# Optimization experiments

Hardware: AMD Instinct MI355X
Metric: run time of the kernel (lower is better)

The kernel has to match this reference:

```python
import jax, jax.numpy as jnp
import numpy as np

CAPACITY = 0.125


def setup_inputs() -> dict:
    key = jax.random.key(0)
    ks = jax.random.split(key, 6)
    b, s, d, dff = 4, 8192, 512, 2048
    x = jax.random.normal(ks[0], (b, s, d), dtype=jnp.float32)
    position_ids = jnp.tile(jnp.arange(s, dtype=jnp.int64)[None, :], (b, 1))
    Wr = jax.random.normal(ks[1], (d,), dtype=jnp.float32) * 0.02
    br = jnp.zeros((1,), dtype=jnp.float32)
    W1 = jax.random.normal(ks[2], (d, dff), dtype=jnp.float32) * 0.02
    b1 = jnp.zeros((dff,), dtype=jnp.float32)
    W2 = jax.random.normal(ks[3], (dff, d), dtype=jnp.float32) * 0.02
    b2 = jnp.zeros((d,), dtype=jnp.float32)
    return {"x": x, "position_ids": position_ids, "Wr": Wr, "br": br,
            "W1": W1, "b1": b1, "W2": W2, "b2": b2}


def reference(x, position_ids, Wr, br, W1, b1, W2, b2):
    b, s, d = x.shape
    # Router: Linear(d, 1) -> squeeze(-1)
    weights = jnp.einsum('bsd,d->bs', x, Wr) + br  # [b, s]
    k = int(CAPACITY * s)
    # Per-batch top-k threshold (k-th largest value)
    top_k_values = jax.lax.top_k(weights, k)[0]  # [b, k], sorted desc
    threshold = top_k_values[:, -1]              # [b]
    selected_mask = weights > threshold[:, None]  # strict >, ties excluded (matches torch)
    # Block: per-token MLP (Linear-GELU-Linear). Per-token ops commute with the
    # gather/scatter, so computing densely and masking is mathematically identical
    # to the original gather -> block -> weighted scatter.
    h = jax.nn.gelu(jnp.einsum('bsd,df->bsf', x, W1) + b1)
    y = jnp.einsum('bsf,fd->bsd', h, W2) + b2
    # processed_tokens (= block_out * router_weight on selected) + x on unselected
    out = jnp.where(selected_mask[..., None], y * weights[..., None], x)
    return out
```

## Files before the change

kernel.cpp:

```cpp
#include <hip/hip_runtime.h>
#include <hip/hip_bf16.h>

#define B_   4
#define S_   8192
#define D_   512
#define DFF_ 2048
#define K_TOP 1024

typedef unsigned short u16;
typedef __attribute__((ext_vector_type(8))) short bf16x8;
typedef __attribute__((ext_vector_type(4))) float floatx4;

__device__ __forceinline__ unsigned f2key(float f){
    unsigned u = __float_as_uint(f);
    return (u & 0x80000000u) ? ~u : (u | 0x80000000u);
}
__device__ __forceinline__ u16 f2b(float f){
    unsigned u = __float_as_uint(f);
    u = (u + 0x7FFFu + ((u >> 16) & 1u)) >> 16;
    return (u16)u;
}
__device__ __forceinline__ float gelu_fast(float v){
    float u = 1.5957691216f * v + 0.0713548162726f * v * v * v;
    float e = __expf(u);
    return v - v / (e + 1.0f);
}
__device__ __forceinline__ void gl_lds16(const void* gptr, void* lptr){
    auto g = (const __attribute__((address_space(1))) unsigned int*)((uintptr_t)gptr);
    auto l = (__attribute__((address_space(3))) unsigned int*)((uintptr_t)lptr);
    __builtin_amdgcn_global_load_lds(g, l, 16, 0, 0);
}


__global__ __launch_bounds__(256) void wts_copy_kernel(
    const float4* __restrict__ x, float4* __restrict__ out,
    const float4* __restrict__ Wr4, const float* __restrict__ br,
    float* __restrict__ w_all, int* __restrict__ count)
{
    if (blockIdx.x == 0 && threadIdx.x == 0) *count = 0;
    const int wv = threadIdx.x >> 6, lane = threadIdx.x & 63;
    const int token = blockIdx.x * 4 + wv;
    const float4* xt = x + (size_t)token * 128;
    float acc = 0.f;
    #pragma unroll
    for (int i = 0; i < 2; i++){
        int j = lane + i * 64;
        float4 v = xt[j];
        out[(size_t)token * 128 + j] = v;
        float4 wvv = Wr4[j];
        acc += v.x*wvv.x + v.y*wvv.y + v.z*wvv.z + v.w*wvv.w;
    }
    #pragma unroll
    for (int off = 32; off > 0; off >>= 1) acc += __shfl_down(acc, off, 64);
    if (lane == 0) w_all[token] = acc + br[0];
}

__global__ __launch_bounds__(1024) void kth_compact_kernel(
    const float4* __restrict__ w_all4, int* __restrict__ count,
    int* __restrict__ idx)
{
    __shared__ unsigned keys[S_];
    __shared__ unsigned hist[16][256];
    __shared__ unsigned suffix[256];
    __shared__ unsigned sprefix;
    __shared__ int sremk;
    const int b = blockIdx.x, tid = threadIdx.x, wv = tid >> 6;
    const float4* row4 = w_all4 + (size_t)b * (S_ / 4);

    #pragma unroll
    for (int i = 0; i < 2; i++){
        int j = tid + i * 1024;
        float4 v = row4[j];
        keys[4*j+0] = f2key(v.x); keys[4*j+1] = f2key(v.y);
        keys[4*j+2] = f2key(v.z); keys[4*j+3] = f2key(v.w);
    }
    if (tid == 0){ sprefix = 0u; sremk = K_TOP; }
    __syncthreads();

    for (int pass = 3; pass >= 0; pass--){
        for (int i = tid; i < 16 * 256; i += 1024) ((unsigned*)hist)[i] = 0u;
        __syncthreads();
        const unsigned mask_hi = (pass == 3) ? 0u : (0xFFFFFFFFu << ((pass + 1) * 8));
        const unsigned pfx = sprefix;
        const int shift = pass * 8;
        #pragma unroll
        for (int i = 0; i < 8; i++){
            unsigned key = keys[tid + i * 1024];
            if ((key & mask_hi) == pfx)
                atomicAdd(&hist[wv][(key >> shift) & 255u], 1u);
        }
        __syncthreads();
        if (tid < 256){
            unsigned s = 0;
            #pragma unroll
            for (int h = 0; h < 16; h++) s += hist[h][tid];
            suffix[tid] = s;
        }
        __syncthreads();
        for (int off = 1; off < 256; off <<= 1){
            unsigned v = 0;
            if (tid < 256 && tid + off < 256) v = suffix[tid + off];
            __syncthreads();
            if (tid < 256) suffix[tid] += v;
            __syncthreads();
        }
        const int remk = sremk;
        __syncthreads();
        if (tid < 256){
            unsigned snext = (tid == 255) ? 0u : suffix[tid + 1];
            if (suffix[tid] >= (unsigned)remk && snext < (unsigned)remk){
                sprefix = pfx | ((unsigned)tid << shift);
                sremk = remk - (int)snext;
            }
        }
        __syncthreads();
    }

    const unsigned thr = sprefix;
    #pragma unroll
    for (int i = 0; i < 8; i++){
        int li = tid + i * 1024;
        if (keys[li] > thr){
            int p = atomicAdd(count, 1);
            idx[p] = b * S_ + li;
        }
    }
}

__global__ __launch_bounds__(256) void gather_kernel(
    const float* __restrict__ x, const int* __restrict__ idx,
    const int* __restrict__ countp, u16* __restrict__ XbT)
{
    const int mt = blockIdx.x, s = blockIdx.y;
    const int cnt = *countp;
    const int cl = threadIdx.x & 15, r16 = threadIdx.x >> 4;
    u16* base = XbT + (size_t)(mt * 4 + s) * 16384;
    #pragma unroll
    for (int it = 0; it < 8; it++){
        int r = r16 + it * 16;
        int mg = mt * 128 + r;
        if (mg < cnt){
            const float* xp = x + (size_t)idx[mg] * D_ + s * 128 + cl * 8;
            float4 v0 = *(const float4*)xp;
            float4 v1 = *(const float4*)(xp + 4);
            bf16x8 bv;
            bv[0]=(short)f2b(v0.x); bv[1]=(short)f2b(v0.y);
            bv[2]=(short)f2b(v0.z); bv[3]=(short)f2b(v0.w);
            bv[4]=(short)f2b(v1.x); bv[5]=(short)f2b(v1.y);
            bv[6]=(short)f2b(v1.z); bv[7]=(short)f2b(v1.w);
            *(bf16x8*)&base[r * 128 + ((cl ^ (r & 15)) << 3)] = bv;
        }
    }
}

__global__ __launch_bounds__(256) void tconv_kernel(
    const float* __restrict__ src, u16* __restrict__ dst, int R, int C)
{
    __shared__ float tile[128][129];
    const int ct = blockIdx.x, ks = blockIdx.y;
    const int tid = threadIdx.x;
    #pragma unroll
    for (int it = 0; it < 64; it++){
        int lin = it * 256 + tid;
        int kk = lin >> 7, nn = lin & 127;
        tile[kk][nn] = src[(size_t)(ks * 128 + kk) * C + ct * 128 + nn];
    }
    __syncthreads();
    u16* base = dst + (size_t)(ct * (R / 128) + ks) * 16384;
    const int r = tid >> 1, h = tid & 1;
    #pragma unroll
    for (int c = 0; c < 8; c++){
        int cl = h * 8 + c;
        bf16x8 bv;
        #pragma unroll
        for (int e = 0; e < 8; e++) bv[e] = (short)f2b(tile[cl * 8 + e][r]);
        *(bf16x8*)&base[r * 128 + ((cl ^ (r & 15)) << 3)] = bv;
    }
}

__global__ __launch_bounds__(256) void ffn1_kernel(
    const u16* __restrict__ XbT, const u16* __restrict__ W1t,
    const int* __restrict__ countp, const float* __restrict__ bias1,
    u16* __restrict__ Ht)
{
    __shared__ __align__(16) u16 As[2][16384];
    __shared__ __align__(16) u16 Bs[2][16384];
    const int tid = threadIdx.x;
    const int cnt = *countp;
    const int mBlk = blockIdx.x, nBlk = blockIdx.y;
    const int lane = tid & 63, w = tid >> 6;
    const int wr = (w >> 1) * 64, wc = (w & 1) * 64;
    const int fr = lane & 15, quad = lane >> 4;

    const char* Ag = (const char*)(XbT + (size_t)mBlk * 4 * 16384) + tid * 16;
    const char* Bg = (const char*)(W1t + (size_t)nBlk * 4 * 16384) + tid * 16;

    #pragma unroll
    for (int i = 0; i < 8; i++){
        gl_lds16(Ag + i*4096, (char*)As[0] + tid*16 + i*4096);
        gl_lds16(Bg + i*4096, (char*)Bs[0] + tid*16 + i*4096);
    }

    floatx4 acc[4][4] = {};
    for (int ksi = 0; ksi < 4; ksi++){
        __syncthreads();
        if (ksi + 1 < 4){
            const char* An = Ag + (size_t)(ksi+1) * 32768;
            const char* Bn = Bg + (size_t)(ksi+1) * 32768;
            char* Al = (char*)As[(ksi+1)&1] + tid*16;
            char* Bl = (char*)Bs[(ksi+1)&1] + tid*16;
            #pragma unroll
            for (int i = 0; i < 8; i++){
                gl_lds16(An + i*4096, Al + i*4096);
                gl_lds16(Bn + i*4096, Bl + i*4096);
            }
        }
        const u16* Ab = As[ksi&1];
        const u16* Bb = Bs[ksi&1];
        #pragma unroll
        for (int ks2 = 0; ks2 < 4; ks2++){
            bf16x8 af[4], bf[4];
            #pragma unroll
            for (int i = 0; i < 4; i++){
                int r = wr + i*16 + fr;
                af[i] = *(const bf16x8*)&Ab[r*128 + (((ks2*4 + quad) ^ (r & 15)) << 3)];
            }
            #pragma unroll
            for (int j = 0; j < 4; j++){
                int r = wc + j*16 + fr;
                bf[j] = *(const bf16x8*)&Bb[r*128 + (((ks2*4 + quad) ^ (r & 15)) << 3)];
            }
            #pragma unroll
            for (int i = 0; i < 4; i++)
                #pragma unroll
                for (int j = 0; j < 4; j++)
                    acc[i][j] = __builtin_amdgcn_mfma_f32_16x16x32_bf16(af[i], bf[j], acc[i][j], 0, 0, 0);
        }
    }

    float bj[4];
    #pragma unroll
    for (int j = 0; j < 4; j++) bj[j] = bias1[nBlk*128 + wc + j*16 + fr];

    __syncthreads();
    u16* Cs = (u16*)As;
    #pragma unroll
    for (int i = 0; i < 4; i++){
        #pragma unroll
        for (int rg = 0; rg < 4; rg++){
            int r = wr + i*16 + quad*4 + rg;
            #pragma unroll
            for (int j = 0; j < 4; j++){
                int col = wc + j*16 + fr;
                float v = gelu_fast(acc[i][j][rg] + bj[j]);
                Cs[r*128 + ((((col >> 3) ^ (r & 15)) << 3) | (col & 7))] = f2b(v);
            }
        }
    }
    __syncthreads();
    const int r = tid >> 1, h = tid & 1;
    int mg = mBlk*128 + r;
    if (mg < cnt){
        u16* dstp = Ht + (((size_t)(mBlk*2 + (r >> 6)) * 16 + nBlk) * 64 + (r & 63)) * 128;
        #pragma unroll
        for (int p = 0; p < 8; p++){
            int pc = h*8 + p;
            *(bf16x8*)&dstp[pc << 3] = *(const bf16x8*)&Cs[r*128 + (pc << 3)];
        }
    }
}

__global__ __launch_bounds__(256) void ffn2_kernel(
    const u16* __restrict__ Ht, const u16* __restrict__ W2t,
    const int* __restrict__ countp, const int* __restrict__ idx,
    const float* __restrict__ w_all, const float* __restrict__ bias2,
    float* __restrict__ out)
{
    __shared__ __align__(16) u16 As[2][8192];
    __shared__ __align__(16) u16 Bs[2][16384];
    const int tid = threadIdx.x;
    const int cnt = *countp;
    const int mBlk = blockIdx.x, nBlk = blockIdx.y;
    const int lane = tid & 63, w = tid >> 6;
    const int wr = (w >> 1) * 32, wc = (w & 1) * 64;
    const int fr = lane & 15, quad = lane >> 4;

    const char* Ag = (const char*)(Ht + (size_t)mBlk * 16 * 8192) + tid * 16;
    const char* Bg = (const char*)(W2t + (size_t)nBlk * 16 * 16384) + tid * 16;

    #pragma unroll
    for (int i = 0; i < 4; i++) gl_lds16(Ag + i*4096, (char*)As[0] + tid*16 + i*4096);
    #pragma unroll
    for (int i = 0; i < 8; i++) gl_lds16(Bg + i*4096, (char*)Bs[0] + tid*16 + i*4096);

    floatx4 acc[2][4] = {};
    for (int ksi = 0; ksi < 16; ksi++){
        __syncthreads();
        if (ksi + 1 < 16){
            const char* An = Ag + (size_t)(ksi+1) * 16384;
            const char* Bn = Bg + (size_t)(ksi+1) * 32768;
            char* Al = (char*)As[(ksi+1)&1] + tid*16;
            char* Bl = (char*)Bs[(ksi+1)&1] + tid*16;
            #pragma unroll
            for (int i = 0; i < 4; i++) gl_lds16(An + i*4096, Al + i*4096);
            #pragma unroll
            for (int i = 0; i < 8; i++) gl_lds16(Bn + i*4096, Bl + i*4096);
        }
        const u16* Ab = As[ksi&1];
        const u16* Bb = Bs[ksi&1];
        #pragma unroll
        for (int ks2 = 0; ks2 < 4; ks2++){
            bf16x8 af[2], bf[4];
            #pragma unroll
            for (int i = 0; i < 2; i++){
                int r = wr + i*16 + fr;
                af[i] = *(const bf16x8*)&Ab[r*128 + (((ks2*4 + quad) ^ (r & 15)) << 3)];
            }
            #pragma unroll
            for (int j = 0; j < 4; j++){
                int r = wc + j*16 + fr;
                bf[j] = *(const bf16x8*)&Bb[r*128 + (((ks2*4 + quad) ^ (r & 15)) << 3)];
            }
            #pragma unroll
            for (int i = 0; i < 2; i++)
                #pragma unroll
                for (int j = 0; j < 4; j++)
                    acc[i][j] = __builtin_amdgcn_mfma_f32_16x16x32_bf16(af[i], bf[j], acc[i][j], 0, 0, 0);
        }
    }

    float bj[4];
    #pragma unroll
    for (int j = 0; j < 4; j++) bj[j] = bias2[nBlk*128 + wc + j*16 + fr];

    __syncthreads();
    float* Cs = (float*)Bs;
    #pragma unroll
    for (int i = 0; i < 2; i++){
        #pragma unroll
        for (int rg = 0; rg < 4; rg++){
            int r = wr + i*16 + quad*4 + rg;
            #pragma unroll
            for (int j = 0; j < 4; j++)
                Cs[r*128 + wc + j*16 + fr] = acc[i][j][rg] + bj[j];
        }
    }
    __syncthreads();
    const int r = tid >> 2, q = tid & 3;
    int mg = mBlk*64 + r;
    if (mg < cnt){
        int token = idx[mg];
        float wt = w_all[token];
        float* op = out + (size_t)token * D_ + nBlk*128 + q*32;
        const float4* cp = (const float4*)&Cs[r*128 + q*32];
        #pragma unroll
        for (int p = 0; p < 8; p++){
            float4 vv = cp[p];
            vv.x *= wt; vv.y *= wt; vv.z *= wt; vv.w *= wt;
            ((float4*)op)[p] = vv;
        }
    }
}

extern "C" void kernel_launch(void* const* d_in, const int* in_sizes, int n_in,
                              void* d_out, int out_size, void* d_ws, size_t ws_size,
                              hipStream_t stream)
{
    const float* x  = (const float*)d_in[0];
    const float* Wr = (const float*)d_in[2];
    const float* br = (const float*)d_in[3];
    const float* W1 = (const float*)d_in[4];
    const float* b1 = (const float*)d_in[5];
    const float* W2 = (const float*)d_in[6];
    const float* b2 = (const float*)d_in[7];
    float* out = (float*)d_out;
    char* ws = (char*)d_ws;

    float* w_all = (float*)(ws + 0);
    int*   count = (int*)  (ws + 131088);
    int*   idx   = (int*)  (ws + 131104);
    u16*   XbT   = (u16*)  (ws + 262144);
    u16*   W1t   = (u16*)  (ws + 4456448);
    u16*   W2t   = (u16*)  (ws + 6553600);
    u16*   Ht    = (u16*)  (ws + 8650752);

    tconv_kernel<<<dim3(DFF_/128, D_/128),  256, 0, stream>>>(W1, W1t, D_, DFF_);
    tconv_kernel<<<dim3(D_/128,  DFF_/128), 256, 0, stream>>>(W2, W2t, DFF_, D_);
    wts_copy_kernel<<<(B_*S_)/4, 256, 0, stream>>>(
        (const float4*)x, (float4*)out, (const float4*)Wr, br, w_all, count);
    kth_compact_kernel<<<B_, 1024, 0, stream>>>((const float4*)w_all, count, idx);
    gather_kernel<<<dim3(32, 4), 256, 0, stream>>>(x, idx, count, XbT);
    ffn1_kernel<<<dim3(32, DFF_/128), 256, 0, stream>>>(XbT, W1t, count, b1, Ht);
    ffn2_kernel<<<dim3(64, D_/128),   256, 0, stream>>>(Ht, W2t, count, idx, w_all, b2, out);
}
```

Before: 204.9 us.

## Fuse weight conversion with router pass, precompute top radix histogram, shrink GEMM LDS stages

```diff
diff --git a/kernel.cpp b/kernel.cpp
--- a/kernel.cpp
+++ b/kernel.cpp
@@ -32,38 +32,83 @@
 }
 
 
-__global__ __launch_bounds__(256) void wts_copy_kernel(
+__global__ __launch_bounds__(256) void prep_kernel(
+    const float* __restrict__ W1, const float* __restrict__ W2,
+    u16* __restrict__ W1t, u16* __restrict__ W2t,
     const float4* __restrict__ x, float4* __restrict__ out,
     const float4* __restrict__ Wr4, const float* __restrict__ br,
-    float* __restrict__ w_all, int* __restrict__ count)
-{
-    if (blockIdx.x == 0 && threadIdx.x == 0) *count = 0;
-    const int wv = threadIdx.x >> 6, lane = threadIdx.x & 63;
-    const int token = blockIdx.x * 4 + wv;
-    const float4* xt = x + (size_t)token * 128;
-    float acc = 0.f;
-    #pragma unroll
-    for (int i = 0; i < 2; i++){
-        int j = lane + i * 64;
-        float4 v = xt[j];
-        out[(size_t)token * 128 + j] = v;
-        float4 wvv = Wr4[j];
-        acc += v.x*wvv.x + v.y*wvv.y + v.z*wvv.z + v.w*wvv.w;
-    }
-    #pragma unroll
-    for (int off = 32; off > 0; off >>= 1) acc += __shfl_down(acc, off, 64);
-    if (lane == 0) w_all[token] = acc + br[0];
+    float* __restrict__ w_all, unsigned* __restrict__ ghist)
+{
+    __shared__ __align__(16) unsigned char shmem[128 * 132 * 2];
+    const int tid = threadIdx.x;
+    const int bx = blockIdx.x;
+    if (bx < 128){
+        const float* src; u16* dst; int R, C, ct, ks;
+        if (bx < 64){ src = W1; dst = W1t; R = D_;   C = DFF_; ct = bx & 15;        ks = bx >> 4; }
+        else        { src = W2; dst = W2t; R = DFF_; C = D_;   ct = (bx - 64) & 3;  ks = (bx - 64) >> 2; }
+        u16 (*tile)[132] = (u16(*)[132])shmem;
+        #pragma unroll
+        for (int it = 0; it < 64; it++){
+            int lin = it * 256 + tid;
+            int kk = lin >> 7, nn = lin & 127;
+            tile[kk][nn] = f2b(src[(size_t)(ks * 128 + kk) * C + ct * 128 + nn]);
+        }
+        __syncthreads();
+        u16* base = dst + (size_t)(ct * (R / 128) + ks) * 16384;
+        const int r = tid >> 1, h = tid & 1;
+        #pragma unroll
+        for (int c = 0; c < 8; c++){
+            int cl = h * 8 + c;
+            bf16x8 bv;
+            #pragma unroll
+            for (int e = 0; e < 8; e++) bv[e] = (short)tile[cl * 8 + e][r];
+            *(bf16x8*)&base[r * 128 + ((cl ^ (r & 15)) << 3)] = bv;
+        }
+    } else {
+        unsigned* hist = (unsigned*)shmem;
+        if (tid < 256) hist[tid] = 0u;
+        __syncthreads();
+        const int wb = bx - 128;
+        const int wv = tid >> 6, lane = tid & 63;
+        const int t0 = wb * 64 + wv * 16;
+        const float brv = br[0];
+        #pragma unroll 2
+        for (int tk = 0; tk < 16; tk++){
+            int token = t0 + tk;
+            const float4* xt = x + (size_t)token * 128;
+            float4* ot = out + (size_t)token * 128;
+            float acc = 0.f;
+            #pragma unroll
+            for (int i = 0; i < 2; i++){
+                int j = lane + i * 64;
+                float4 v = xt[j];
+                ot[j] = v;
+                float4 wv4 = Wr4[j];
+                acc += v.x*wv4.x + v.y*wv4.y + v.z*wv4.z + v.w*wv4.w;
+            }
+            #pragma unroll
+            for (int off = 32; off > 0; off >>= 1) acc += __shfl_down(acc, off, 64);
+            if (lane == 0){
+                float wt = acc + brv;
+                w_all[token] = wt;
+                atomicAdd(&hist[f2key(wt) >> 24], 1u);
+            }
+        }
+        __syncthreads();
+        if (tid < 256) ghist[wb * 256 + tid] = hist[tid];
+    }
 }
 
 __global__ __launch_bounds__(1024) void kth_compact_kernel(
-    const float4* __restrict__ w_all4, int* __restrict__ count,
-    int* __restrict__ idx)
+    const float4* __restrict__ w_all4, const unsigned* __restrict__ ghist,
+    int* __restrict__ counts, int* __restrict__ idx)
 {
     __shared__ unsigned keys[S_];
     __shared__ unsigned hist[16][256];
     __shared__ unsigned suffix[256];
     __shared__ unsigned sprefix;
     __shared__ int sremk;
+    __shared__ int lbase;
     const int b = blockIdx.x, tid = threadIdx.x, wv = tid >> 6;
     const float4* row4 = w_all4 + (size_t)b * (S_ / 4);
 
@@ -74,13 +119,35 @@
         keys[4*j+0] = f2key(v.x); keys[4*j+1] = f2key(v.y);
         keys[4*j+2] = f2key(v.z); keys[4*j+3] = f2key(v.w);
     }
-    if (tid == 0){ sprefix = 0u; sremk = K_TOP; }
-    __syncthreads();
-
-    for (int pass = 3; pass >= 0; pass--){
+    if (tid < 256){
+        unsigned s = 0;
+        const unsigned* gh = ghist + (size_t)(b * 128) * 256 + tid;
+        #pragma unroll 8
+        for (int j = 0; j < 128; j++) s += gh[j * 256];
+        suffix[tid] = s;
+    }
+    if (tid == 0) lbase = 0;
+    __syncthreads();
+    for (int off = 1; off < 256; off <<= 1){
+        unsigned v = 0;
+        if (tid < 256 && tid + off < 256) v = suffix[tid + off];
+        __syncthreads();
+        if (tid < 256) suffix[tid] += v;
+        __syncthreads();
+    }
+    if (tid < 256){
+        unsigned snext = (tid == 255) ? 0u : suffix[tid + 1];
+        if (suffix[tid] >= (unsigned)K_TOP && snext < (unsigned)K_TOP){
+            sprefix = ((unsigned)tid) << 24;
+            sremk = K_TOP - (int)snext;
+        }
+    }
+    __syncthreads();
+
+    for (int pass = 2; pass >= 0; pass--){
         for (int i = tid; i < 16 * 256; i += 1024) ((unsigned*)hist)[i] = 0u;
         __syncthreads();
-        const unsigned mask_hi = (pass == 3) ? 0u : (0xFFFFFFFFu << ((pass + 1) * 8));
+        const unsigned mask_hi = 0xFFFFFFFFu << ((pass + 1) * 8);
         const unsigned pfx = sprefix;
         const int shift = pass * 8;
         #pragma unroll
@@ -120,26 +187,35 @@
     #pragma unroll
     for (int i = 0; i < 8; i++){
         int li = tid + i * 1024;
-        if (keys[li] > thr){
-            int p = atomicAdd(count, 1);
-            idx[p] = b * S_ + li;
-        }
-    }
+        bool sel = keys[li] > thr;
+        unsigned long long m = __ballot(sel);
+        int wtot = (int)__popcll(m);
+        if (wtot){
+            int woff = 0;
+            if ((tid & 63) == 0) woff = atomicAdd(&lbase, wtot);
+            woff = __shfl(woff, 0, 64);
+            if (sel){
+                int pos = woff + (int)__popcll(m & ((1ull << (tid & 63)) - 1ull));
+                idx[b * 1024 + pos] = b * S_ + li;
+            }
+        }
+    }
+    __syncthreads();
+    if (tid == 0) counts[b] = lbase;
 }
 
 __global__ __launch_bounds__(256) void gather_kernel(
     const float* __restrict__ x, const int* __restrict__ idx,
-    const int* __restrict__ countp, u16* __restrict__ XbT)
+    const int* __restrict__ counts, u16* __restrict__ XbT)
 {
     const int mt = blockIdx.x, s = blockIdx.y;
-    const int cnt = *countp;
     const int cl = threadIdx.x & 15, r16 = threadIdx.x >> 4;
     u16* base = XbT + (size_t)(mt * 4 + s) * 16384;
     #pragma unroll
     for (int it = 0; it < 8; it++){
         int r = r16 + it * 16;
         int mg = mt * 128 + r;
-        if (mg < cnt){
+        if ((mg & 1023) < counts[mg >> 10]){
             const float* xp = x + (size_t)idx[mg] * D_ + s * 128 + cl * 8;
             float4 v0 = *(const float4*)xp;
             float4 v1 = *(const float4*)(xp + 4);
@@ -153,82 +229,59 @@
     }
 }
 
-__global__ __launch_bounds__(256) void tconv_kernel(
-    const float* __restrict__ src, u16* __restrict__ dst, int R, int C)
-{
-    __shared__ float tile[128][129];
-    const int ct = blockIdx.x, ks = blockIdx.y;
-    const int tid = threadIdx.x;
-    #pragma unroll
-    for (int it = 0; it < 64; it++){
-        int lin = it * 256 + tid;
-        int kk = lin >> 7, nn = lin & 127;
-        tile[kk][nn] = src[(size_t)(ks * 128 + kk) * C + ct * 128 + nn];
-    }
-    __syncthreads();
-    u16* base = dst + (size_t)(ct * (R / 128) + ks) * 16384;
-    const int r = tid >> 1, h = tid & 1;
-    #pragma unroll
-    for (int c = 0; c < 8; c++){
-        int cl = h * 8 + c;
-        bf16x8 bv;
-        #pragma unroll
-        for (int e = 0; e < 8; e++) bv[e] = (short)f2b(tile[cl * 8 + e][r]);
-        *(bf16x8*)&base[r * 128 + ((cl ^ (r & 15)) << 3)] = bv;
-    }
-}
-
 __global__ __launch_bounds__(256) void ffn1_kernel(
     const u16* __restrict__ XbT, const u16* __restrict__ W1t,
-    const int* __restrict__ countp, const float* __restrict__ bias1,
+    const int* __restrict__ counts, const float* __restrict__ bias1,
     u16* __restrict__ Ht)
 {
-    __shared__ __align__(16) u16 As[2][16384];
-    __shared__ __align__(16) u16 Bs[2][16384];
+    __shared__ __align__(16) u16 smem[32768];
     const int tid = threadIdx.x;
-    const int cnt = *countp;
     const int mBlk = blockIdx.x, nBlk = blockIdx.y;
     const int lane = tid & 63, w = tid >> 6;
     const int wr = (w >> 1) * 64, wc = (w & 1) * 64;
     const int fr = lane & 15, quad = lane >> 4;
 
-    const char* Ag = (const char*)(XbT + (size_t)mBlk * 4 * 16384) + tid * 16;
-    const char* Bg = (const char*)(W1t + (size_t)nBlk * 4 * 16384) + tid * 16;
-
-    #pragma unroll
-    for (int i = 0; i < 8; i++){
-        gl_lds16(Ag + i*4096, (char*)As[0] + tid*16 + i*4096);
-        gl_lds16(Bg + i*4096, (char*)Bs[0] + tid*16 + i*4096);
-    }
+    const char* Abase = (const char*)(XbT + (size_t)mBlk * 4 * 16384);
+    const char* Bbase = (const char*)(W1t + (size_t)nBlk * 4 * 16384);
+    char* Al0 = (char*)smem + tid * 16;
+    char* Bl0 = (char*)(smem + 16384) + tid * 16;
+    const int rr0 = tid >> 3, pp = tid & 7;
+
+    auto stage = [&](const char* gbase, char* lb, int hs){
+        const char* s0 = gbase + (size_t)(hs >> 1) * 32768;
+        const int h = hs & 1;
+        #pragma unroll
+        for (int i = 0; i < 4; i++){
+            int r = rr0 + i * 32;
+            int pg = pp | (((h ^ (r >> 3)) & 1) << 3);
+            gl_lds16(s0 + r * 256 + pg * 16, lb + i * 4096);
+        }
+    };
+
+    stage(Abase, Al0, 0);
+    stage(Bbase, Bl0, 0);
 
     floatx4 acc[4][4] = {};
-    for (int ksi = 0; ksi < 4; ksi++){
-        __syncthreads();
-        if (ksi + 1 < 4){
-            const char* An = Ag + (size_t)(ksi+1) * 32768;
-            const char* Bn = Bg + (size_t)(ksi+1) * 32768;
-            char* Al = (char*)As[(ksi+1)&1] + tid*16;
-            char* Bl = (char*)Bs[(ksi+1)&1] + tid*16;
-            #pragma unroll
-            for (int i = 0; i < 8; i++){
-                gl_lds16(An + i*4096, Al + i*4096);
-                gl_lds16(Bn + i*4096, Bl + i*4096);
-            }
-        }
-        const u16* Ab = As[ksi&1];
-        const u16* Bb = Bs[ksi&1];
-        #pragma unroll
-        for (int ks2 = 0; ks2 < 4; ks2++){
+    for (int hs = 0; hs < 8; hs++){
+        __syncthreads();
+        if (hs + 1 < 8){
+            stage(Abase, Al0 + ((hs + 1) & 1) * 16384, hs + 1);
+            stage(Bbase, Bl0 + ((hs + 1) & 1) * 16384, hs + 1);
+        }
+        const u16* Ab = smem + (hs & 1) * 8192;
+        const u16* Bb = smem + 16384 + (hs & 1) * 8192;
+        #pragma unroll
+        for (int ks2 = 0; ks2 < 2; ks2++){
             bf16x8 af[4], bf[4];
             #pragma unroll
             for (int i = 0; i < 4; i++){
-                int r = wr + i*16 + fr;
-                af[i] = *(const bf16x8*)&Ab[r*128 + (((ks2*4 + quad) ^ (r & 15)) << 3)];
+                int r = wr + i * 16 + fr;
+                af[i] = *(const bf16x8*)&Ab[r * 64 + (((ks2 * 4 + quad) ^ (r & 7)) << 3)];
             }
             #pragma unroll
             for (int j = 0; j < 4; j++){
-                int r = wc + j*16 + fr;
-                bf[j] = *(const bf16x8*)&Bb[r*128 + (((ks2*4 + quad) ^ (r & 15)) << 3)];
+                int r = wc + j * 16 + fr;
+                bf[j] = *(const bf16x8*)&Bb[r * 64 + (((ks2 * 4 + quad) ^ (r & 7)) << 3)];
             }
             #pragma unroll
             for (int i = 0; i < 4; i++)
@@ -240,86 +293,97 @@
 
     float bj[4];
     #pragma unroll
-    for (int j = 0; j < 4; j++) bj[j] = bias1[nBlk*128 + wc + j*16 + fr];
-
-    __syncthreads();
-    u16* Cs = (u16*)As;
+    for (int j = 0; j < 4; j++) bj[j] = bias1[nBlk * 128 + wc + j * 16 + fr];
+
+    __syncthreads();
+    u16* Cs = smem;
     #pragma unroll
     for (int i = 0; i < 4; i++){
         #pragma unroll
         for (int rg = 0; rg < 4; rg++){
-            int r = wr + i*16 + quad*4 + rg;
+            int r = wr + i * 16 + quad * 4 + rg;
             #pragma unroll
             for (int j = 0; j < 4; j++){
-                int col = wc + j*16 + fr;
+                int col = wc + j * 16 + fr;
                 float v = gelu_fast(acc[i][j][rg] + bj[j]);
-                Cs[r*128 + ((((col >> 3) ^ (r & 15)) << 3) | (col & 7))] = f2b(v);
+                Cs[r * 128 + ((((col >> 3) ^ (r & 15)) << 3) | (col & 7))] = f2b(v);
             }
         }
     }
     __syncthreads();
     const int r = tid >> 1, h = tid & 1;
-    int mg = mBlk*128 + r;
-    if (mg < cnt){
-        u16* dstp = Ht + (((size_t)(mBlk*2 + (r >> 6)) * 16 + nBlk) * 64 + (r & 63)) * 128;
+    int mg = mBlk * 128 + r;
+    if ((mg & 1023) < counts[mg >> 10]){
+        u16* dstp = Ht + (((size_t)(mBlk * 2 + (r >> 6)) * 16 + nBlk) * 64 + (r & 63)) * 128;
         #pragma unroll
         for (int p = 0; p < 8; p++){
-            int pc = h*8 + p;
-            *(bf16x8*)&dstp[pc << 3] = *(const bf16x8*)&Cs[r*128 + (pc << 3)];
+            int pc = h * 8 + p;
+            *(bf16x8*)&dstp[pc << 3] = *(const bf16x8*)&Cs[r * 128 + (pc << 3)];
         }
     }
 }
 
 __global__ __launch_bounds__(256) void ffn2_kernel(
     const u16* __restrict__ Ht, const u16* __restrict__ W2t,
-    const int* __restrict__ countp, const int* __restrict__ idx,
+    const int* __restrict__ counts, const int* __restrict__ idx,
     const float* __restrict__ w_all, const float* __restrict__ bias2,
     float* __restrict__ out)
 {
-    __shared__ __align__(16) u16 As[2][8192];
-    __shared__ __align__(16) u16 Bs[2][16384];
+    __shared__ __align__(16) u16 smem[24576];
     const int tid = threadIdx.x;
-    const int cnt = *countp;
     const int mBlk = blockIdx.x, nBlk = blockIdx.y;
     const int lane = tid & 63, w = tid >> 6;
     const int wr = (w >> 1) * 32, wc = (w & 1) * 64;
     const int fr = lane & 15, quad = lane >> 4;
 
-    const char* Ag = (const char*)(Ht + (size_t)mBlk * 16 * 8192) + tid * 16;
-    const char* Bg = (const char*)(W2t + (size_t)nBlk * 16 * 16384) + tid * 16;
-
-    #pragma unroll
-    for (int i = 0; i < 4; i++) gl_lds16(Ag + i*4096, (char*)As[0] + tid*16 + i*4096);
-    #pragma unroll
-    for (int i = 0; i < 8; i++) gl_lds16(Bg + i*4096, (char*)Bs[0] + tid*16 + i*4096);
-
+    const char* Abase = (const char*)(Ht + (size_t)mBlk * 16 * 8192);
+    const char* Bbase = (const char*)(W2t + (size_t)nBlk * 16 * 16384);
+    char* Al0 = (char*)smem + tid * 16;
+    char* Bl0 = (char*)(smem + 8192) + tid * 16;
+    const int rr0 = tid >> 3, pp = tid & 7;
+
+    auto stageA = [&](int buf, int hs){
+        const char* s0 = Abase + (size_t)(hs >> 1) * 16384;
+        const int h = hs & 1;
+        char* l = Al0 + buf * 8192;
+        #pragma unroll
+        for (int i = 0; i < 2; i++){
+            int r = rr0 + i * 32;
+            int pg = pp | (((h ^ (r >> 3)) & 1) << 3);
+            gl_lds16(s0 + r * 256 + pg * 16, l + i * 4096);
+        }
+    };
+    auto stageB = [&](int buf, int hs){
+        const char* s0 = Bbase + (size_t)(hs >> 1) * 32768;
+        const int h = hs & 1;
+        char* l = Bl0 + buf * 16384;
+        #pragma unroll
+        for (int i = 0; i < 4; i++){
+            int r = rr0 + i * 32;
+            int pg = pp | (((h ^ (r >> 3)) & 1) << 3);
+            gl_lds16(s0 + r * 256 + pg * 16, l + i * 4096);
+        }
+    };
+
+    stageA(0, 0); stageB(0, 0);
     floatx4 acc[2][4] = {};
-    for (int ksi = 0; ksi < 16; ksi++){
-        __syncthreads();
-        if (ksi + 1 < 16){
-            const char* An = Ag + (size_t)(ksi+1) * 16384;
-            const char* Bn = Bg + (size_t)(ksi+1) * 32768;
-            char* Al = (char*)As[(ksi+1)&1] + tid*16;
-            char* Bl = (char*)Bs[(ksi+1)&1] + tid*16;
-            #pragma unroll
-            for (int i = 0; i < 4; i++) gl_lds16(An + i*4096, Al + i*4096);
-            #pragma unroll
-            for (int i = 0; i < 8; i++) gl_lds16(Bn + i*4096, Bl + i*4096);
-        }
-        const u16* Ab = As[ksi&1];
-        const u16* Bb = Bs[ksi&1];
-        #pragma unroll
-        for (int ks2 = 0; ks2 < 4; ks2++){
+    for (int hs = 0; hs < 32; hs++){
+        __syncthreads();
+        if (hs + 1 < 32){ stageA((hs + 1) & 1, hs + 1); stageB((hs + 1) & 1, hs + 1); }
+        const u16* Ab = smem + (hs & 1) * 4096;
+        const u16* Bb = smem + 8192 + (hs & 1) * 8192;
+        #pragma unroll
+        for (int ks2 = 0; ks2 < 2; ks2++){
             bf16x8 af[2], bf[4];
             #pragma unroll
             for (int i = 0; i < 2; i++){
-                int r = wr + i*16 + fr;
-                af[i] = *(const bf16x8*)&Ab[r*128 + (((ks2*4 + quad) ^ (r & 15)) << 3)];
+                int r = wr + i * 16 + fr;
+                af[i] = *(const bf16x8*)&Ab[r * 64 + (((ks2 * 4 + quad) ^ (r & 7)) << 3)];
             }
             #pragma unroll
             for (int j = 0; j < 4; j++){
-                int r = wc + j*16 + fr;
-                bf[j] = *(const bf16x8*)&Bb[r*128 + (((ks2*4 + quad) ^ (r & 15)) << 3)];
+                int r = wc + j * 16 + fr;
+                bf[j] = *(const bf16x8*)&Bb[r * 64 + (((ks2 * 4 + quad) ^ (r & 7)) << 3)];
             }
             #pragma unroll
             for (int i = 0; i < 2; i++)
@@ -331,28 +395,28 @@
 
     float bj[4];
     #pragma unroll
-    for (int j = 0; j < 4; j++) bj[j] = bias2[nBlk*128 + wc + j*16 + fr];
-
-    __syncthreads();
-    float* Cs = (float*)Bs;
+    for (int j = 0; j < 4; j++) bj[j] = bias2[nBlk * 128 + wc + j * 16 + fr];
+
+    __syncthreads();
+    float* Cs = (float*)smem;
     #pragma unroll
     for (int i = 0; i < 2; i++){
         #pragma unroll
         for (int rg = 0; rg < 4; rg++){
-            int r = wr + i*16 + quad*4 + rg;
+            int r = wr + i * 16 + quad * 4 + rg;
             #pragma unroll
             for (int j = 0; j < 4; j++)
-                Cs[r*128 + wc + j*16 + fr] = acc[i][j][rg] + bj[j];
+                Cs[r * 128 + wc + j * 16 + fr] = acc[i][j][rg] + bj[j];
         }
     }
     __syncthreads();
     const int r = tid >> 2, q = tid & 3;
-    int mg = mBlk*64 + r;
-    if (mg < cnt){
+    int mg = mBlk * 64 + r;
+    if ((mg & 1023) < counts[mg >> 10]){
         int token = idx[mg];
         float wt = w_all[token];
-        float* op = out + (size_t)token * D_ + nBlk*128 + q*32;
-        const float4* cp = (const float4*)&Cs[r*128 + q*32];
+        float* op = out + (size_t)token * D_ + nBlk * 128 + q * 32;
+        const float4* cp = (const float4*)&Cs[r * 128 + q * 32];
         #pragma unroll
         for (int p = 0; p < 8; p++){
             float4 vv = cp[p];
@@ -376,20 +440,21 @@
     float* out = (float*)d_out;
     char* ws = (char*)d_ws;
 
-    float* w_all = (float*)(ws + 0);
-    int*   count = (int*)  (ws + 131088);
-    int*   idx   = (int*)  (ws + 131104);
-    u16*   XbT   = (u16*)  (ws + 262144);
-    u16*   W1t   = (u16*)  (ws + 4456448);
-    u16*   W2t   = (u16*)  (ws + 6553600);
-    u16*   Ht    = (u16*)  (ws + 8650752);
-
-    tconv_kernel<<<dim3(DFF_/128, D_/128),  256, 0, stream>>>(W1, W1t, D_, DFF_);
-    tconv_kernel<<<dim3(D_/128,  DFF_/128), 256, 0, stream>>>(W2, W2t, DFF_, D_);
-    wts_copy_kernel<<<(B_*S_)/4, 256, 0, stream>>>(
-        (const float4*)x, (float4*)out, (const float4*)Wr, br, w_all, count);
-    kth_compact_kernel<<<B_, 1024, 0, stream>>>((const float4*)w_all, count, idx);
-    gather_kernel<<<dim3(32, 4), 256, 0, stream>>>(x, idx, count, XbT);
-    ffn1_kernel<<<dim3(32, DFF_/128), 256, 0, stream>>>(XbT, W1t, count, b1, Ht);
-    ffn2_kernel<<<dim3(64, D_/128),   256, 0, stream>>>(Ht, W2t, count, idx, w_all, b2, out);
-}
+    float*    w_all  = (float*)   (ws + 0);
+    int*      counts = (int*)     (ws + 131072);
+    int*      idx    = (int*)     (ws + 131136);
+    unsigned* ghist  = (unsigned*)(ws + 163840);
+    u16*      XbT    = (u16*)     (ws + 720896);
+    u16*      W1t    = (u16*)     (ws + 4915200);
+    u16*      W2t    = (u16*)     (ws + 7012352);
+    u16*      Ht     = (u16*)     (ws + 9109504);
+
+    prep_kernel<<<640, 256, 0, stream>>>(
+        W1, W2, W1t, W2t, (const float4*)x, (float4*)out,
+        (const float4*)Wr, br, w_all, ghist);
+    kth_compact_kernel<<<B_, 1024, 0, stream>>>(
+        (const float4*)w_all, ghist, counts, idx);
+    gather_kernel<<<dim3(32, 4), 256, 0, stream>>>(x, idx, counts, XbT);
+    ffn1_kernel<<<dim3(32, DFF_/128), 256, 0, stream>>>(XbT, W1t, counts, b1, Ht);
+    ffn2_kernel<<<dim3(64, D_/128),   256, 0, stream>>>(Ht, W2t, counts, idx, w_all, b2, out);
+}
```

After: 193.6 us. -5.5%, faster.
